# Kernel optimization log

Hardware: AMD Instinct MI355X
Metric: run time of the kernel (lower is better)

## Reference

```python
import jax, jax.numpy as jnp
import numpy as np

B, N, D, H = 32, 2048, 1024, 16
HD = D // H


def setup_inputs() -> dict:
    key = jax.random.key(0)
    ks = jax.random.split(key, 12)
    s = 1.0 / np.sqrt(D)  # xavier-ish scale for square projections
    return {
        "z": jax.random.normal(ks[0], (B, N, D), dtype=jnp.float32),
        "mask": jax.random.bernoulli(ks[1], 0.9, (B, N)),
        "query": jax.random.normal(ks[2], (1, 1, D), dtype=jnp.float32) * s,
        "w_q": jax.random.normal(ks[3], (D, D), dtype=jnp.float32) * s,
        "w_k": jax.random.normal(ks[4], (D, D), dtype=jnp.float32) * s,
        "w_v": jax.random.normal(ks[5], (D, D), dtype=jnp.float32) * s,
        "b_q": jnp.zeros((D,), dtype=jnp.float32),
        "b_k": jnp.zeros((D,), dtype=jnp.float32),
        "b_v": jnp.zeros((D,), dtype=jnp.float32),
        "w_o": jax.random.normal(ks[6], (D, D), dtype=jnp.float32) * s,
        "b_o": jnp.zeros((D,), dtype=jnp.float32),
    }


def reference(z, mask, query, w_q, w_k, w_v, b_q, b_k, b_v, w_o, b_o):
    # mask: True = valid key. Guarantee at least one valid key per row
    # (torch code sets mask[b, 0] = True for all-False rows).
    all_false = ~jnp.any(mask, axis=1)                 # [B]
    valid = mask.at[:, 0].set(mask[:, 0] | all_false)  # [B, N]

    # Projections (PyTorch Linear: x @ W.T + b)
    q = (query @ w_q.T + b_q).reshape(H, HD)           # single shared query -> [H, HD]
    k = (z @ w_k.T + b_k).reshape(B, N, H, HD)
    v = (z @ w_v.T + b_v).reshape(B, N, H, HD)

    scale = 1.0 / jnp.sqrt(jnp.asarray(HD, dtype=z.dtype))
    scores = jnp.einsum('hd,bnhd->bhn', q, k) * scale  # [B, H, N]
    scores = jnp.where(valid[:, None, :], scores, -jnp.inf)
    attn = jax.nn.softmax(scores, axis=-1)             # [B, H, N]

    pooled = jnp.einsum('bhn,bnhd->bhd', attn, v).reshape(B, D)
    return pooled @ w_o.T + b_o                        # [B, D]
```

## Files before the change

### kernel.cpp

```cpp
#include <hip/hip_runtime.h>
#include <hip/hip_bf16.h>
#include <stdint.h>

#define B_ 32
#define N_ 2048
#define D_ 1024
#define H_ 16

#define NT 16
#define RPAD 1028

typedef __attribute__((ext_vector_type(8))) short short8;
typedef __attribute__((ext_vector_type(4))) float f32x4;

__device__ __forceinline__ unsigned short f2bf(float x) {
    unsigned u = __float_as_uint(x);
    u += 0x7FFFu + ((u >> 16) & 1u);
    return (unsigned short)(u >> 16);
}
__device__ __forceinline__ float bflo(unsigned u) { return __uint_as_float(u << 16); }

__device__ __forceinline__ short8 cvt8(float4 a, float4 b) {
    union { __hip_bfloat162 h[4]; short8 s; } u;
    u.h[0] = __float22bfloat162_rn(make_float2(a.x, a.y));
    u.h[1] = __float22bfloat162_rn(make_float2(a.z, a.w));
    u.h[2] = __float22bfloat162_rn(make_float2(b.x, b.y));
    u.h[3] = __float22bfloat162_rn(make_float2(b.z, b.w));
    return u.s;
}

__global__ __launch_bounds__(256) void prep_k(const float* __restrict__ query,
        const float* __restrict__ w_q, const float* __restrict__ b_q,
        const float* __restrict__ w_k, const int* __restrict__ mask,
        unsigned short* __restrict__ rAf, int* __restrict__ any_ws) {
    __shared__ __align__(16) float qv[1024];
    __shared__ float qp[64][5];
    __shared__ float qh[64];
    __shared__ int wf[4];
    int bx = blockIdx.x, t = threadIdx.x;
    if (bx < 64) {
        int h = bx >> 2, dg = bx & 3;
        *(float4*)&qv[4 * t] = *(const float4*)&query[4 * t];
        __syncthreads();
        {
            int j = t >> 2, sub = t & 3;
            const float4* wq4 = (const float4*)(w_q + (size_t)(h * 64 + j) * 1024);
            const float4* qv4 = (const float4*)qv;
            float a = 0.f;
            #pragma unroll 8
            for (int kk = 0; kk < 64; kk++) {
                float4 wv = wq4[sub * 64 + kk];
                float4 vv = qv4[sub * 64 + kk];
                a += wv.x * vv.x + wv.y * vv.y + wv.z * vv.z + wv.w * vv.w;
            }
            qp[j][sub] = a;
        }
        __syncthreads();
        if (t < 64)
            qh[t] = qp[t][0] + qp[t][1] + qp[t][2] + qp[t][3] + b_q[h * 64 + t];
        __syncthreads();
        int d = dg * 256 + t;
        float acc = 0.f;
        #pragma unroll 8
        for (int j = 0; j < 64; j++)
            acc += qh[j] * w_k[(size_t)(h * 64 + j) * 1024 + d];
        acc *= 0.125f;
        int i = d >> 5, fq = (d >> 3) & 3, jj = d & 7;
        int lane = (fq << 4) | h;
        rAf[(size_t)(i * 64 + lane) * 8 + jj] = f2bf(acc);
    } else {
        int b = bx - 64;
        int v = 0;
        for (int k = 0; k < 8; k++) v |= mask[b * N_ + k * 256 + t];
        unsigned long long bal = __ballot(v != 0);
        int w = t >> 6;
        if ((t & 63) == 0) wf[w] = (bal != 0ull) ? 1 : 0;
        __syncthreads();
        if (t == 0) any_ws[b] = wf[0] | wf[1] | wf[2] | wf[3];
    }
}

__global__ __launch_bounds__(256, 1) void main_k(const float* __restrict__ z,
        const int* __restrict__ mask, const int* __restrict__ any_ws,
        const unsigned short* __restrict__ rAf,
        unsigned short* __restrict__ part, float* __restrict__ l_part) {
    __shared__ __align__(16) float zt[2][16 * RPAD];
    __shared__ __align__(16) float Ew[4][16][16];
    int bx = blockIdx.x, t = threadIdx.x;
    int b = bx >> 3, c = bx & 7;
    int n0 = c * 256;
    int w = t >> 6, l = t & 63;
    int frow = l & 15, fquad = l >> 4;
    int anyb = any_ws[b];

    short8 rA[32];
    {
        const short8* rA8 = (const short8*)rAf;
        #pragma unroll
        for (int i = 0; i < 32; i++) rA[i] = rA8[i * 64 + l];
    }
    const float* zb = z + (size_t)b * N_ * D_ + n0 * D_;

    float4 ctx[16];
    #pragma unroll
    for (int h = 0; h < 16; h++) ctx[h] = make_float4(0.f, 0.f, 0.f, 0.f);
    float l4[4] = {0.f, 0.f, 0.f, 0.f};

    #define STAGE(p, tile)                                                        \
        {                                                                         \
            const float* gsrc = zb + (size_t)(tile) * 16 * D_ + w * 256 + l * 4;  \
            float* ldst = &zt[(p)][w * 256];                                      \
            _Pragma("unroll")                                                     \
            for (int r = 0; r < 16; r++) {                                        \
                __builtin_amdgcn_global_load_lds(                                 \
                    (const __attribute__((address_space(1))) unsigned int*)       \
                        (gsrc + (size_t)r * D_),                                  \
                    (__attribute__((address_space(3))) unsigned int*)             \
                        (ldst + r * RPAD),                                        \
                    16, 0, 0);                                                    \
            }                                                                     \
        }

    STAGE(0, 0)
    __syncthreads();

    for (int it = 0; it < NT; it++) {
        int p = it & 1;
        if (it + 1 < NT) STAGE(p ^ 1, it + 1)

        f32x4 a0 = {0.f,0.f,0.f,0.f}, a1 = {0.f,0.f,0.f,0.f};
        f32x4 a2 = {0.f,0.f,0.f,0.f}, a3 = {0.f,0.f,0.f,0.f};
        const float* brow = &zt[p][frow * RPAD + fquad * 8];
        #pragma unroll
        for (int i = 0; i < 32; i += 4) {
            float4 z00 = *(const float4*)(brow + (i + 0) * 32);
            float4 z01 = *(const float4*)(brow + (i + 0) * 32 + 4);
            float4 z10 = *(const float4*)(brow + (i + 1) * 32);
            float4 z11 = *(const float4*)(brow + (i + 1) * 32 + 4);
            float4 z20 = *(const float4*)(brow + (i + 2) * 32);
            float4 z21 = *(const float4*)(brow + (i + 2) * 32 + 4);
            float4 z30 = *(const float4*)(brow + (i + 3) * 32);
            float4 z31 = *(const float4*)(brow + (i + 3) * 32 + 4);
            a0 = __builtin_amdgcn_mfma_f32_16x16x32_bf16(rA[i + 0], cvt8(z00, z01), a0, 0, 0, 0);
            a1 = __builtin_amdgcn_mfma_f32_16x16x32_bf16(rA[i + 1], cvt8(z10, z11), a1, 0, 0, 0);
            a2 = __builtin_amdgcn_mfma_f32_16x16x32_bf16(rA[i + 2], cvt8(z20, z21), a2, 0, 0, 0);
            a3 = __builtin_amdgcn_mfma_f32_16x16x32_bf16(rA[i + 3], cvt8(z30, z31), a3, 0, 0, 0);
        }
        f32x4 acc = a0 + a1 + a2 + a3;

        {
            int gn = n0 + it * 16 + frow;
            bool valid = (mask[b * N_ + gn] != 0) || (gn == 0 && anyb == 0);
            float e0 = valid ? __expf(acc[0]) : 0.f;
            float e1 = valid ? __expf(acc[1]) : 0.f;
            float e2 = valid ? __expf(acc[2]) : 0.f;
            float e3 = valid ? __expf(acc[3]) : 0.f;
            l4[0] += e0; l4[1] += e1; l4[2] += e2; l4[3] += e3;
            *(float4*)&Ew[w][frow][fquad * 4] = make_float4(e0, e1, e2, e3);
        }

        {
            const float* zcol = &zt[p][w * 256 + 4 * l];
            #pragma unroll 4
            for (int r = 0; r < 16; r++) {
                float4 zr = *(const float4*)(zcol + r * RPAD);
                const float4* er4 = (const float4*)&Ew[w][r][0];
                float4 e0 = er4[0], e1 = er4[1], e2 = er4[2], e3 = er4[3];
                ctx[0].x  += e0.x * zr.x; ctx[0].y  += e0.x * zr.y; ctx[0].z  += e0.x * zr.z; ctx[0].w  += e0.x * zr.w;
                ctx[1].x  += e0.y * zr.x; ctx[1].y  += e0.y * zr.y; ctx[1].z  += e0.y * zr.z; ctx[1].w  += e0.y * zr.w;
                ctx[2].x  += e0.z * zr.x; ctx[2].y  += e0.z * zr.y; ctx[2].z  += e0.z * zr.z; ctx[2].w  += e0.z * zr.w;
                ctx[3].x  += e0.w * zr.x; ctx[3].y  += e0.w * zr.y; ctx[3].z  += e0.w * zr.z; ctx[3].w  += e0.w * zr.w;
                ctx[4].x  += e1.x * zr.x; ctx[4].y  += e1.x * zr.y; ctx[4].z  += e1.x * zr.z; ctx[4].w  += e1.x * zr.w;
                ctx[5].x  += e1.y * zr.x; ctx[5].y  += e1.y * zr.y; ctx[5].z  += e1.y * zr.z; ctx[5].w  += e1.y * zr.w;
                ctx[6].x  += e1.z * zr.x; ctx[6].y  += e1.z * zr.y; ctx[6].z  += e1.z * zr.z; ctx[6].w  += e1.z * zr.w;
                ctx[7].x  += e1.w * zr.x; ctx[7].y  += e1.w * zr.y; ctx[7].z  += e1.w * zr.z; ctx[7].w  += e1.w * zr.w;
                ctx[8].x  += e2.x * zr.x; ctx[8].y  += e2.x * zr.y; ctx[8].z  += e2.x * zr.z; ctx[8].w  += e2.x * zr.w;
                ctx[9].x  += e2.y * zr.x; ctx[9].y  += e2.y * zr.y; ctx[9].z  += e2.y * zr.z; ctx[9].w  += e2.y * zr.w;
                ctx[10].x += e2.z * zr.x; ctx[10].y += e2.z * zr.y; ctx[10].z += e2.z * zr.z; ctx[10].w += e2.z * zr.w;
                ctx[11].x += e2.w * zr.x; ctx[11].y += e2.w * zr.y; ctx[11].z += e2.w * zr.z; ctx[11].w += e2.w * zr.w;
                ctx[12].x += e3.x * zr.x; ctx[12].y += e3.x * zr.y; ctx[12].z += e3.x * zr.z; ctx[12].w += e3.x * zr.w;
                ctx[13].x += e3.y * zr.x; ctx[13].y += e3.y * zr.y; ctx[13].z += e3.y * zr.z; ctx[13].w += e3.y * zr.w;
                ctx[14].x += e3.z * zr.x; ctx[14].y += e3.z * zr.y; ctx[14].z += e3.z * zr.z; ctx[14].w += e3.z * zr.w;
                ctx[15].x += e3.w * zr.x; ctx[15].y += e3.w * zr.y; ctx[15].z += e3.w * zr.z; ctx[15].w += e3.w * zr.w;
            }
        }
        __syncthreads();
    }

    {
        unsigned short* pp = part + (size_t)bx * 16 * 1024 + w * 256 + 4 * l;
        #pragma unroll
        for (int h = 0; h < 16; h++) {
            ushort4 o;
            o.x = f2bf(ctx[h].x); o.y = f2bf(ctx[h].y);
            o.z = f2bf(ctx[h].z); o.w = f2bf(ctx[h].w);
            *(ushort4*)(pp + h * 1024) = o;
        }
    }
    if (w == 0) {
        #pragma unroll
        for (int r = 0; r < 4; r++) {
            float v = l4[r];
            v += __shfl_xor(v, 1, 64);
            v += __shfl_xor(v, 2, 64);
            v += __shfl_xor(v, 4, 64);
            v += __shfl_xor(v, 8, 64);
            if (frow == 0) l_part[bx * 16 + fquad * 4 + r] = v;
        }
    }
}

__global__ __launch_bounds__(256) void gemv_wv_k(const unsigned short* __restrict__ part,
        const float* __restrict__ l_part, const float* __restrict__ w_v,
        const float* __restrict__ b_v, float* __restrict__ pooled) {
    __shared__ __align__(16) float vlds[1024];
    int bx = blockIdx.x, t = threadIdx.x;
    int b = bx >> 4, h = bx & 15;
    float L = 0.f;
    #pragma unroll
    for (int cc = 0; cc < 8; cc++) L += l_part[(b * 8 + cc) * 16 + h];
    float rL = 1.f / L;
    float sx = 0.f, sy = 0.f, sz = 0.f, sw = 0.f;
    #pragma unroll
    for (int cc = 0; cc < 8; cc++) {
        const ushort4* p4 = (const ushort4*)&part[(((size_t)(b * 8 + cc)) * 16 + h) * 1024];
        ushort4 u = p4[t];
        sx += bflo(u.x); sy += bflo(u.y); sz += bflo(u.z); sw += bflo(u.w);
    }
    *(float4*)&vlds[4 * t] = make_float4(sx * rL, sy * rL, sz * rL, sw * rL);
    __syncthreads();
    int w = t >> 6, l = t & 63;
    const float4* v4 = (const float4*)vlds;
    float* orow = pooled + (size_t)b * 1024;
    #pragma unroll
    for (int s0 = 0; s0 < 16; s0 += 4) {
        int jb = h * 64 + w * 16 + s0;
        float a0 = 0.f, a1 = 0.f, a2 = 0.f, a3 = 0.f;
        #pragma unroll
        for (int kk = 0; kk < 4; kk++) {
            float4 v = v4[kk * 64 + l];
            float4 w0 = *(const float4*)&w_v[(size_t)(jb + 0) * 1024 + (kk * 64 + l) * 4];
            float4 w1 = *(const float4*)&w_v[(size_t)(jb + 1) * 1024 + (kk * 64 + l) * 4];
            float4 w2 = *(const float4*)&w_v[(size_t)(jb + 2) * 1024 + (kk * 64 + l) * 4];
            float4 w3 = *(const float4*)&w_v[(size_t)(jb + 3) * 1024 + (kk * 64 + l) * 4];
            a0 += w0.x * v.x + w0.y * v.y + w0.z * v.z + w0.w * v.w;
            a1 += w1.x * v.x + w1.y * v.y + w1.z * v.z + w1.w * v.w;
            a2 += w2.x * v.x + w2.y * v.y + w2.z * v.z + w2.w * v.w;
            a3 += w3.x * v.x + w3.y * v.y + w3.z * v.z + w3.w * v.w;
        }
        #pragma unroll
        for (int m = 32; m >= 1; m >>= 1) {
            a0 += __shfl_xor(a0, m, 64); a1 += __shfl_xor(a1, m, 64);
            a2 += __shfl_xor(a2, m, 64); a3 += __shfl_xor(a3, m, 64);
        }
        if (l == 0) {
            orow[jb + 0] = a0 + b_v[jb + 0];
            orow[jb + 1] = a1 + b_v[jb + 1];
            orow[jb + 2] = a2 + b_v[jb + 2];
            orow[jb + 3] = a3 + b_v[jb + 3];
        }
    }
}

__global__ __launch_bounds__(256) void gemv_wo_k(const float* __restrict__ pooled,
        const float* __restrict__ w_o, const float* __restrict__ b_o,
        float* __restrict__ out) {
    __shared__ __align__(16) float vlds[1024];
    int bx = blockIdx.x, t = threadIdx.x;
    int b = bx >> 4, q = bx & 15;
    *(float4*)&vlds[4 * t] = *(const float4*)&pooled[(size_t)b * 1024 + 4 * t];
    __syncthreads();
    int w = t >> 6, l = t & 63;
    const float4* v4 = (const float4*)vlds;
    float* orow = out + (size_t)b * 1024;
    #pragma unroll
    for (int s0 = 0; s0 < 16; s0 += 4) {
        int jb = q * 64 + w * 16 + s0;
        float a0 = 0.f, a1 = 0.f, a2 = 0.f, a3 = 0.f;
        #pragma unroll
        for (int kk = 0; kk < 4; kk++) {
            float4 v = v4[kk * 64 + l];
            float4 w0 = *(const float4*)&w_o[(size_t)(jb + 0) * 1024 + (kk * 64 + l) * 4];
            float4 w1 = *(const float4*)&w_o[(size_t)(jb + 1) * 1024 + (kk * 64 + l) * 4];
            float4 w2 = *(const float4*)&w_o[(size_t)(jb + 2) * 1024 + (kk * 64 + l) * 4];
            float4 w3 = *(const float4*)&w_o[(size_t)(jb + 3) * 1024 + (kk * 64 + l) * 4];
            a0 += w0.x * v.x + w0.y * v.y + w0.z * v.z + w0.w * v.w;
            a1 += w1.x * v.x + w1.y * v.y + w1.z * v.z + w1.w * v.w;
            a2 += w2.x * v.x + w2.y * v.y + w2.z * v.z + w2.w * v.w;
            a3 += w3.x * v.x + w3.y * v.y + w3.z * v.z + w3.w * v.w;
        }
        #pragma unroll
        for (int m = 32; m >= 1; m >>= 1) {
            a0 += __shfl_xor(a0, m, 64); a1 += __shfl_xor(a1, m, 64);
            a2 += __shfl_xor(a2, m, 64); a3 += __shfl_xor(a3, m, 64);
        }
        if (l == 0) {
            orow[jb + 0] = a0 + b_o[jb + 0];
            orow[jb + 1] = a1 + b_o[jb + 1];
            orow[jb + 2] = a2 + b_o[jb + 2];
            orow[jb + 3] = a3 + b_o[jb + 3];
        }
    }
}

extern "C" void kernel_launch(void* const* d_in, const int* in_sizes, int n_in,
                              void* d_out, int out_size, void* d_ws, size_t ws_size,
                              hipStream_t stream) {
    const float* z     = (const float*)d_in[0];
    const int*   mask  = (const int*)d_in[1];
    const float* query = (const float*)d_in[2];
    const float* w_q   = (const float*)d_in[3];
    const float* w_k   = (const float*)d_in[4];
    const float* w_v   = (const float*)d_in[5];
    const float* b_q   = (const float*)d_in[6];
    const float* b_v   = (const float*)d_in[8];
    const float* w_o   = (const float*)d_in[9];
    const float* b_o   = (const float*)d_in[10];
    float* out = (float*)d_out;

    char* ws = (char*)d_ws;
    unsigned short* rAf    = (unsigned short*)(ws + 0);
    int*            any_ws = (int*)(ws + 32768);
    float*          l_part = (float*)(ws + 40960);
    float*          pooled = (float*)(ws + 65536);
    unsigned short* part   = (unsigned short*)(ws + 1048576);

    prep_k<<<96, 256, 0, stream>>>(query, w_q, b_q, w_k, mask, rAf, any_ws);
    main_k<<<256, 256, 0, stream>>>(z, mask, any_ws, rAf, part, l_part);
    gemv_wv_k<<<512, 256, 0, stream>>>(part, l_part, w_v, b_v, pooled);
    gemv_wo_k<<<512, 256, 0, stream>>>(pooled, w_o, b_o, out);
}
```

Baseline: 457.5 us.

## Stage z tiles as bf16 in LDS via register prefetch, double grid occupancy

Replaces the direct global-to-LDS fp32 staging with register-held global loads that are converted to bf16 once and written to LDS in three chunks interleaved with the MFMA and context phases. This halves the LDS footprint, so two blocks fit per CU, and the grid doubles to 512 blocks of 128 keys each. Mask values are also cached in LDS, and the downstream gemv reduces over 16 partials instead of 8. The cost is higher register pressure from the prefetch buffers, plus bf16 rounding of z in the value-weighted sum, which was fp32 before.

```diff
diff --git a/kernel.cpp b/kernel.cpp
--- a/kernel.cpp
+++ b/kernel.cpp
@@ -7,8 +7,8 @@
 #define D_ 1024
 #define H_ 16
 
-#define NT 16
-#define RPAD 1028
+#define NT 8
+#define RPB 1032
 
 typedef __attribute__((ext_vector_type(8))) short short8;
 typedef __attribute__((ext_vector_type(4))) float f32x4;
@@ -80,15 +80,16 @@
     }
 }
 
-__global__ __launch_bounds__(256, 1) void main_k(const float* __restrict__ z,
+__global__ __launch_bounds__(256, 2) void main_k(const float* __restrict__ z,
         const int* __restrict__ mask, const int* __restrict__ any_ws,
         const unsigned short* __restrict__ rAf,
         unsigned short* __restrict__ part, float* __restrict__ l_part) {
-    __shared__ __align__(16) float zt[2][16 * RPAD];
-    __shared__ __align__(16) float Ew[4][16][16];
+    __shared__ __align__(16) unsigned short ztb[2][16 * RPB];
+    __shared__ __align__(16) float Ew[4][16][20];
+    __shared__ int mlds[128];
     int bx = blockIdx.x, t = threadIdx.x;
-    int b = bx >> 3, c = bx & 7;
-    int n0 = c * 256;
+    int b = bx >> 4, c = bx & 15;
+    int n0 = c * 128;
     int w = t >> 6, l = t & 63;
     int frow = l & 15, fquad = l >> 4;
     int anyb = any_ws[b];
@@ -99,58 +100,81 @@
         #pragma unroll
         for (int i = 0; i < 32; i++) rA[i] = rA8[i * 64 + l];
     }
-    const float* zb = z + (size_t)b * N_ * D_ + n0 * D_;
+    const float* zb = z + (size_t)b * N_ * D_ + (size_t)n0 * D_;
+
+    if (t < 128) mlds[t] = mask[b * N_ + n0 + t];
 
     float4 ctx[16];
     #pragma unroll
     for (int h = 0; h < 16; h++) ctx[h] = make_float4(0.f, 0.f, 0.f, 0.f);
     float l4[4] = {0.f, 0.f, 0.f, 0.f};
 
-    #define STAGE(p, tile)                                                        \
+    float4 ga[4], gb[4], gc[8];
+    #define ISSUE4(g, tile, rb)                                                   \
         {                                                                         \
-            const float* gsrc = zb + (size_t)(tile) * 16 * D_ + w * 256 + l * 4;  \
-            float* ldst = &zt[(p)][w * 256];                                      \
-            _Pragma("unroll")                                                     \
-            for (int r = 0; r < 16; r++) {                                        \
-                __builtin_amdgcn_global_load_lds(                                 \
-                    (const __attribute__((address_space(1))) unsigned int*)       \
-                        (gsrc + (size_t)r * D_),                                  \
-                    (__attribute__((address_space(3))) unsigned int*)             \
-                        (ldst + r * RPAD),                                        \
-                    16, 0, 0);                                                    \
-            }                                                                     \
-        }
-
-    STAGE(0, 0)
+            const float4* src = (const float4*)(zb + (size_t)(tile) * 16 * D_ +   \
+                                                (size_t)((rb) + w) * D_);         \
+            g[0] = src[2 * l];       g[1] = src[2 * l + 1];                       \
+            g[2] = src[2 * (l + 64)]; g[3] = src[2 * (l + 64) + 1];               \
+        }
+    #define WRITE4(g, pp, rb)                                                     \
+        {                                                                         \
+            unsigned short* dst = &ztb[(pp)][((rb) + w) * RPB];                   \
+            *(short8*)(dst + l * 8) = cvt8(g[0], g[1]);                           \
+            *(short8*)(dst + (l + 64) * 8) = cvt8(g[2], g[3]);                    \
+        }
+    #define ISSUE8(g, tile)                                                       \
+        {                                                                         \
+            const float4* s0 = (const float4*)(zb + (size_t)(tile) * 16 * D_ +    \
+                                               (size_t)(8 + 2 * w) * D_);         \
+            const float4* s1 = (const float4*)(zb + (size_t)(tile) * 16 * D_ +    \
+                                               (size_t)(9 + 2 * w) * D_);         \
+            g[0] = s0[2 * l];       g[1] = s0[2 * l + 1];                         \
+            g[2] = s0[2 * (l + 64)]; g[3] = s0[2 * (l + 64) + 1];                 \
+            g[4] = s1[2 * l];       g[5] = s1[2 * l + 1];                         \
+            g[6] = s1[2 * (l + 64)]; g[7] = s1[2 * (l + 64) + 1];                 \
+        }
+    #define WRITE8(g, pp)                                                         \
+        {                                                                         \
+            unsigned short* d0 = &ztb[(pp)][(8 + 2 * w) * RPB];                   \
+            unsigned short* d1 = &ztb[(pp)][(9 + 2 * w) * RPB];                   \
+            *(short8*)(d0 + l * 8) = cvt8(g[0], g[1]);                            \
+            *(short8*)(d0 + (l + 64) * 8) = cvt8(g[2], g[3]);                     \
+            *(short8*)(d1 + l * 8) = cvt8(g[4], g[5]);                            \
+            *(short8*)(d1 + (l + 64) * 8) = cvt8(g[6], g[7]);                     \
+        }
+
+    ISSUE4(ga, 0, 0)  WRITE4(ga, 0, 0)
+    ISSUE4(gb, 0, 4)  WRITE4(gb, 0, 4)
+    ISSUE8(gc, 0)     WRITE8(gc, 0)
     __syncthreads();
 
     for (int it = 0; it < NT; it++) {
         int p = it & 1;
-        if (it + 1 < NT) STAGE(p ^ 1, it + 1)
+        bool nx = (it + 1 < NT);
+        if (nx) ISSUE4(ga, it + 1, 0)
 
         f32x4 a0 = {0.f,0.f,0.f,0.f}, a1 = {0.f,0.f,0.f,0.f};
         f32x4 a2 = {0.f,0.f,0.f,0.f}, a3 = {0.f,0.f,0.f,0.f};
-        const float* brow = &zt[p][frow * RPAD + fquad * 8];
+        const unsigned short* brow = &ztb[p][frow * RPB + fquad * 8];
         #pragma unroll
         for (int i = 0; i < 32; i += 4) {
-            float4 z00 = *(const float4*)(brow + (i + 0) * 32);
-            float4 z01 = *(const float4*)(brow + (i + 0) * 32 + 4);
-            float4 z10 = *(const float4*)(brow + (i + 1) * 32);
-            float4 z11 = *(const float4*)(brow + (i + 1) * 32 + 4);
-            float4 z20 = *(const float4*)(brow + (i + 2) * 32);
-            float4 z21 = *(const float4*)(brow + (i + 2) * 32 + 4);
-            float4 z30 = *(const float4*)(brow + (i + 3) * 32);
-            float4 z31 = *(const float4*)(brow + (i + 3) * 32 + 4);
-            a0 = __builtin_amdgcn_mfma_f32_16x16x32_bf16(rA[i + 0], cvt8(z00, z01), a0, 0, 0, 0);
-            a1 = __builtin_amdgcn_mfma_f32_16x16x32_bf16(rA[i + 1], cvt8(z10, z11), a1, 0, 0, 0);
-            a2 = __builtin_amdgcn_mfma_f32_16x16x32_bf16(rA[i + 2], cvt8(z20, z21), a2, 0, 0, 0);
-            a3 = __builtin_amdgcn_mfma_f32_16x16x32_bf16(rA[i + 3], cvt8(z30, z31), a3, 0, 0, 0);
+            short8 b0 = *(const short8*)(brow + (i + 0) * 32);
+            short8 b1 = *(const short8*)(brow + (i + 1) * 32);
+            short8 b2 = *(const short8*)(brow + (i + 2) * 32);
+            short8 b3 = *(const short8*)(brow + (i + 3) * 32);
+            a0 = __builtin_amdgcn_mfma_f32_16x16x32_bf16(rA[i + 0], b0, a0, 0, 0, 0);
+            a1 = __builtin_amdgcn_mfma_f32_16x16x32_bf16(rA[i + 1], b1, a1, 0, 0, 0);
+            a2 = __builtin_amdgcn_mfma_f32_16x16x32_bf16(rA[i + 2], b2, a2, 0, 0, 0);
+            a3 = __builtin_amdgcn_mfma_f32_16x16x32_bf16(rA[i + 3], b3, a3, 0, 0, 0);
         }
         f32x4 acc = a0 + a1 + a2 + a3;
+
+        if (nx) { WRITE4(ga, p ^ 1, 0)  ISSUE4(gb, it + 1, 4) }
 
         {
             int gn = n0 + it * 16 + frow;
-            bool valid = (mask[b * N_ + gn] != 0) || (gn == 0 && anyb == 0);
+            bool valid = (mlds[it * 16 + frow] != 0) || (gn == 0 && anyb == 0);
             float e0 = valid ? __expf(acc[0]) : 0.f;
             float e1 = valid ? __expf(acc[1]) : 0.f;
             float e2 = valid ? __expf(acc[2]) : 0.f;
@@ -159,31 +183,37 @@
             *(float4*)&Ew[w][frow][fquad * 4] = make_float4(e0, e1, e2, e3);
         }
 
-        {
-            const float* zcol = &zt[p][w * 256 + 4 * l];
-            #pragma unroll 4
-            for (int r = 0; r < 16; r++) {
-                float4 zr = *(const float4*)(zcol + r * RPAD);
-                const float4* er4 = (const float4*)&Ew[w][r][0];
-                float4 e0 = er4[0], e1 = er4[1], e2 = er4[2], e3 = er4[3];
-                ctx[0].x  += e0.x * zr.x; ctx[0].y  += e0.x * zr.y; ctx[0].z  += e0.x * zr.z; ctx[0].w  += e0.x * zr.w;
-                ctx[1].x  += e0.y * zr.x; ctx[1].y  += e0.y * zr.y; ctx[1].z  += e0.y * zr.z; ctx[1].w  += e0.y * zr.w;
-                ctx[2].x  += e0.z * zr.x; ctx[2].y  += e0.z * zr.y; ctx[2].z  += e0.z * zr.z; ctx[2].w  += e0.z * zr.w;
-                ctx[3].x  += e0.w * zr.x; ctx[3].y  += e0.w * zr.y; ctx[3].z  += e0.w * zr.z; ctx[3].w  += e0.w * zr.w;
-                ctx[4].x  += e1.x * zr.x; ctx[4].y  += e1.x * zr.y; ctx[4].z  += e1.x * zr.z; ctx[4].w  += e1.x * zr.w;
-                ctx[5].x  += e1.y * zr.x; ctx[5].y  += e1.y * zr.y; ctx[5].z  += e1.y * zr.z; ctx[5].w  += e1.y * zr.w;
-                ctx[6].x  += e1.z * zr.x; ctx[6].y  += e1.z * zr.y; ctx[6].z  += e1.z * zr.z; ctx[6].w  += e1.z * zr.w;
-                ctx[7].x  += e1.w * zr.x; ctx[7].y  += e1.w * zr.y; ctx[7].z  += e1.w * zr.z; ctx[7].w  += e1.w * zr.w;
-                ctx[8].x  += e2.x * zr.x; ctx[8].y  += e2.x * zr.y; ctx[8].z  += e2.x * zr.z; ctx[8].w  += e2.x * zr.w;
-                ctx[9].x  += e2.y * zr.x; ctx[9].y  += e2.y * zr.y; ctx[9].z  += e2.y * zr.z; ctx[9].w  += e2.y * zr.w;
-                ctx[10].x += e2.z * zr.x; ctx[10].y += e2.z * zr.y; ctx[10].z += e2.z * zr.z; ctx[10].w += e2.z * zr.w;
-                ctx[11].x += e2.w * zr.x; ctx[11].y += e2.w * zr.y; ctx[11].z += e2.w * zr.z; ctx[11].w += e2.w * zr.w;
-                ctx[12].x += e3.x * zr.x; ctx[12].y += e3.x * zr.y; ctx[12].z += e3.x * zr.z; ctx[12].w += e3.x * zr.w;
-                ctx[13].x += e3.y * zr.x; ctx[13].y += e3.y * zr.y; ctx[13].z += e3.y * zr.z; ctx[13].w += e3.y * zr.w;
-                ctx[14].x += e3.z * zr.x; ctx[14].y += e3.z * zr.y; ctx[14].z += e3.z * zr.z; ctx[14].w += e3.z * zr.w;
-                ctx[15].x += e3.w * zr.x; ctx[15].y += e3.w * zr.y; ctx[15].z += e3.w * zr.z; ctx[15].w += e3.w * zr.w;
+        const unsigned short* zcol = &ztb[p][w * 256 + 4 * l];
+        #define CTXROW(r)                                                         \
+            {                                                                     \
+                ushort4 u = *(const ushort4*)(zcol + (r) * RPB);                  \
+                float zx = bflo(u.x), zy = bflo(u.y);                             \
+                float zz = bflo(u.z), zw = bflo(u.w);                             \
+                const float4* er4 = (const float4*)&Ew[w][(r)][0];                \
+                float4 e0 = er4[0], e1 = er4[1], e2 = er4[2], e3 = er4[3];        \
+                ctx[0].x  += e0.x * zx; ctx[0].y  += e0.x * zy; ctx[0].z  += e0.x * zz; ctx[0].w  += e0.x * zw; \
+                ctx[1].x  += e0.y * zx; ctx[1].y  += e0.y * zy; ctx[1].z  += e0.y * zz; ctx[1].w  += e0.y * zw; \
+                ctx[2].x  += e0.z * zx; ctx[2].y  += e0.z * zy; ctx[2].z  += e0.z * zz; ctx[2].w  += e0.z * zw; \
+                ctx[3].x  += e0.w * zx; ctx[3].y  += e0.w * zy; ctx[3].z  += e0.w * zz; ctx[3].w  += e0.w * zw; \
+                ctx[4].x  += e1.x * zx; ctx[4].y  += e1.x * zy; ctx[4].z  += e1.x * zz; ctx[4].w  += e1.x * zw; \
+                ctx[5].x  += e1.y * zx; ctx[5].y  += e1.y * zy; ctx[5].z  += e1.y * zz; ctx[5].w  += e1.y * zw; \
+                ctx[6].x  += e1.z * zx; ctx[6].y  += e1.z * zy; ctx[6].z  += e1.z * zz; ctx[6].w  += e1.z * zw; \
+                ctx[7].x  += e1.w * zx; ctx[7].y  += e1.w * zy; ctx[7].z  += e1.w * zz; ctx[7].w  += e1.w * zw; \
+                ctx[8].x  += e2.x * zx; ctx[8].y  += e2.x * zy; ctx[8].z  += e2.x * zz; ctx[8].w  += e2.x * zw; \
+                ctx[9].x  += e2.y * zx; ctx[9].y  += e2.y * zy; ctx[9].z  += e2.y * zz; ctx[9].w  += e2.y * zw; \
+                ctx[10].x += e2.z * zx; ctx[10].y += e2.z * zy; ctx[10].z += e2.z * zz; ctx[10].w += e2.z * zw; \
+                ctx[11].x += e2.w * zx; ctx[11].y += e2.w * zy; ctx[11].z += e2.w * zz; ctx[11].w += e2.w * zw; \
+                ctx[12].x += e3.x * zx; ctx[12].y += e3.x * zy; ctx[12].z += e3.x * zz; ctx[12].w += e3.x * zw; \
+                ctx[13].x += e3.y * zx; ctx[13].y += e3.y * zy; ctx[13].z += e3.y * zz; ctx[13].w += e3.y * zw; \
+                ctx[14].x += e3.z * zx; ctx[14].y += e3.z * zy; ctx[14].z += e3.z * zz; ctx[14].w += e3.z * zw; \
+                ctx[15].x += e3.w * zx; ctx[15].y += e3.w * zy; ctx[15].z += e3.w * zz; ctx[15].w += e3.w * zw; \
             }
-        }
+        #pragma unroll
+        for (int r = 0; r < 8; r++) CTXROW(r)
+        if (nx) { WRITE4(gb, p ^ 1, 4)  ISSUE8(gc, it + 1) }
+        #pragma unroll
+        for (int r = 8; r < 16; r++) CTXROW(r)
+        if (nx) WRITE8(gc, p ^ 1)
         __syncthreads();
     }
 
@@ -218,12 +248,12 @@
     int b = bx >> 4, h = bx & 15;
     float L = 0.f;
     #pragma unroll
-    for (int cc = 0; cc < 8; cc++) L += l_part[(b * 8 + cc) * 16 + h];
+    for (int cc = 0; cc < 16; cc++) L += l_part[(b * 16 + cc) * 16 + h];
     float rL = 1.f / L;
     float sx = 0.f, sy = 0.f, sz = 0.f, sw = 0.f;
     #pragma unroll
-    for (int cc = 0; cc < 8; cc++) {
-        const ushort4* p4 = (const ushort4*)&part[(((size_t)(b * 8 + cc)) * 16 + h) * 1024];
+    for (int cc = 0; cc < 16; cc++) {
+        const ushort4* p4 = (const ushort4*)&part[(((size_t)(b * 16 + cc)) * 16 + h) * 1024];
         ushort4 u = p4[t];
         sx += bflo(u.x); sy += bflo(u.y); sz += bflo(u.z); sw += bflo(u.w);
     }
@@ -321,12 +351,12 @@
     char* ws = (char*)d_ws;
     unsigned short* rAf    = (unsigned short*)(ws + 0);
     int*            any_ws = (int*)(ws + 32768);
-    float*          l_part = (float*)(ws + 40960);
-    float*          pooled = (float*)(ws + 65536);
+    float*          l_part = (float*)(ws + 36864);
+    float*          pooled = (float*)(ws + 131072);
     unsigned short* part   = (unsigned short*)(ws + 1048576);
 
     prep_k<<<96, 256, 0, stream>>>(query, w_q, b_q, w_k, mask, rAf, any_ws);
-    main_k<<<256, 256, 0, stream>>>(z, mask, any_ws, rAf, part, l_part);
+    main_k<<<512, 256, 0, stream>>>(z, mask, any_ws, rAf, part, l_part);
     gemv_wv_k<<<512, 256, 0, stream>>>(part, l_part, w_v, b_v, pooled);
     gemv_wo_k<<<512, 256, 0, stream>>>(pooled, w_o, b_o, out);
 }
```

New measurement: 902.0 us. 1.97x slower.

## Double main kernel waves to split context accumulation and cache mask in LDS

Applied to the files above, without the earlier changes.

The main attention kernel goes from 256 to 512 threads per block, so each wave accumulates the weighted context over 128 feature columns instead of 256. This halves the per-thread FMA work and the register footprint of the context accumulators. The staging loop is remapped so each wave copies two full rows of the z tile, and the per-block mask slice is preloaded into shared memory instead of being read from global memory every iteration. In exchange, every wave still computes the full score MFMA redundantly, so that work doubles per block. The tighter launch bound also risks register spills, given the 32 resident bf16 query fragments.

```diff
diff --git a/kernel.cpp b/kernel.cpp
--- a/kernel.cpp
+++ b/kernel.cpp
@@ -80,12 +80,13 @@
     }
 }
 
-__global__ __launch_bounds__(256, 1) void main_k(const float* __restrict__ z,
+__global__ __launch_bounds__(512, 2) void main_k(const float* __restrict__ z,
         const int* __restrict__ mask, const int* __restrict__ any_ws,
         const unsigned short* __restrict__ rAf,
         unsigned short* __restrict__ part, float* __restrict__ l_part) {
     __shared__ __align__(16) float zt[2][16 * RPAD];
-    __shared__ __align__(16) float Ew[4][16][16];
+    __shared__ __align__(16) float Ew[8][16][16];
+    __shared__ int mlds[256];
     int bx = blockIdx.x, t = threadIdx.x;
     int b = bx >> 3, c = bx & 7;
     int n0 = c * 256;
@@ -99,25 +100,32 @@
         #pragma unroll
         for (int i = 0; i < 32; i++) rA[i] = rA8[i * 64 + l];
     }
-    const float* zb = z + (size_t)b * N_ * D_ + n0 * D_;
-
-    float4 ctx[16];
-    #pragma unroll
-    for (int h = 0; h < 16; h++) ctx[h] = make_float4(0.f, 0.f, 0.f, 0.f);
+    const float* zb = z + (size_t)b * N_ * D_ + (size_t)n0 * D_;
+
+    if (t < 256) mlds[t] = mask[b * N_ + n0 + t];
+
+    float2 ctx[16];
+    #pragma unroll
+    for (int h = 0; h < 16; h++) ctx[h] = make_float2(0.f, 0.f);
     float l4[4] = {0.f, 0.f, 0.f, 0.f};
 
     #define STAGE(p, tile)                                                        \
         {                                                                         \
-            const float* gsrc = zb + (size_t)(tile) * 16 * D_ + w * 256 + l * 4;  \
-            float* ldst = &zt[(p)][w * 256];                                      \
             _Pragma("unroll")                                                     \
-            for (int r = 0; r < 16; r++) {                                        \
-                __builtin_amdgcn_global_load_lds(                                 \
-                    (const __attribute__((address_space(1))) unsigned int*)       \
-                        (gsrc + (size_t)r * D_),                                  \
-                    (__attribute__((address_space(3))) unsigned int*)             \
-                        (ldst + r * RPAD),                                        \
-                    16, 0, 0);                                                    \
+            for (int rr = 0; rr < 2; rr++) {                                      \
+                int row = 2 * w + rr;                                             \
+                const float* gsrc = zb + (size_t)(tile) * 16 * D_ +               \
+                                    (size_t)row * D_ + l * 4;                     \
+                float* ldst = &zt[(p)][row * RPAD];                               \
+                _Pragma("unroll")                                                 \
+                for (int q = 0; q < 4; q++) {                                     \
+                    __builtin_amdgcn_global_load_lds(                             \
+                        (const __attribute__((address_space(1))) unsigned int*)   \
+                            (gsrc + q * 256),                                     \
+                        (__attribute__((address_space(3))) unsigned int*)         \
+                            (ldst + q * 256),                                     \
+                        16, 0, 0);                                                \
+                }                                                                 \
             }                                                                     \
         }
 
@@ -150,7 +158,7 @@
 
         {
             int gn = n0 + it * 16 + frow;
-            bool valid = (mask[b * N_ + gn] != 0) || (gn == 0 && anyb == 0);
+            bool valid = (mlds[it * 16 + frow] != 0) || (gn == 0 && anyb == 0);
             float e0 = valid ? __expf(acc[0]) : 0.f;
             float e1 = valid ? __expf(acc[1]) : 0.f;
             float e2 = valid ? __expf(acc[2]) : 0.f;
@@ -160,41 +168,40 @@
         }
 
         {
-            const float* zcol = &zt[p][w * 256 + 4 * l];
+            const float* zcol = &zt[p][w * 128 + 2 * l];
             #pragma unroll 4
             for (int r = 0; r < 16; r++) {
-                float4 zr = *(const float4*)(zcol + r * RPAD);
+                float2 zr = *(const float2*)(zcol + r * RPAD);
                 const float4* er4 = (const float4*)&Ew[w][r][0];
                 float4 e0 = er4[0], e1 = er4[1], e2 = er4[2], e3 = er4[3];
-                ctx[0].x  += e0.x * zr.x; ctx[0].y  += e0.x * zr.y; ctx[0].z  += e0.x * zr.z; ctx[0].w  += e0.x * zr.w;
-                ctx[1].x  += e0.y * zr.x; ctx[1].y  += e0.y * zr.y; ctx[1].z  += e0.y * zr.z; ctx[1].w  += e0.y * zr.w;
-                ctx[2].x  += e0.z * zr.x; ctx[2].y  += e0.z * zr.y; ctx[2].z  += e0.z * zr.z; ctx[2].w  += e0.z * zr.w;
-                ctx[3].x  += e0.w * zr.x; ctx[3].y  += e0.w * zr.y; ctx[3].z  += e0.w * zr.z; ctx[3].w  += e0.w * zr.w;
-                ctx[4].x  += e1.x * zr.x; ctx[4].y  += e1.x * zr.y; ctx[4].z  += e1.x * zr.z; ctx[4].w  += e1.x * zr.w;
-                ctx[5].x  += e1.y * zr.x; ctx[5].y  += e1.y * zr.y; ctx[5].z  += e1.y * zr.z; ctx[5].w  += e1.y * zr.w;
-                ctx[6].x  += e1.z * zr.x; ctx[6].y  += e1.z * zr.y; ctx[6].z  += e1.z * zr.z; ctx[6].w  += e1.z * zr.w;
-                ctx[7].x  += e1.w * zr.x; ctx[7].y  += e1.w * zr.y; ctx[7].z  += e1.w * zr.z; ctx[7].w  += e1.w * zr.w;
-                ctx[8].x  += e2.x * zr.x; ctx[8].y  += e2.x * zr.y; ctx[8].z  += e2.x * zr.z; ctx[8].w  += e2.x * zr.w;
-                ctx[9].x  += e2.y * zr.x; ctx[9].y  += e2.y * zr.y; ctx[9].z  += e2.y * zr.z; ctx[9].w  += e2.y * zr.w;
-                ctx[10].x += e2.z * zr.x; ctx[10].y += e2.z * zr.y; ctx[10].z += e2.z * zr.z; ctx[10].w += e2.z * zr.w;
-                ctx[11].x += e2.w * zr.x; ctx[11].y += e2.w * zr.y; ctx[11].z += e2.w * zr.z; ctx[11].w += e2.w * zr.w;
-                ctx[12].x += e3.x * zr.x; ctx[12].y += e3.x * zr.y; ctx[12].z += e3.x * zr.z; ctx[12].w += e3.x * zr.w;
-                ctx[13].x += e3.y * zr.x; ctx[13].y += e3.y * zr.y; ctx[13].z += e3.y * zr.z; ctx[13].w += e3.y * zr.w;
-                ctx[14].x += e3.z * zr.x; ctx[14].y += e3.z * zr.y; ctx[14].z += e3.z * zr.z; ctx[14].w += e3.z * zr.w;
-                ctx[15].x += e3.w * zr.x; ctx[15].y += e3.w * zr.y; ctx[15].z += e3.w * zr.z; ctx[15].w += e3.w * zr.w;
+                ctx[0].x  += e0.x * zr.x; ctx[0].y  += e0.x * zr.y;
+                ctx[1].x  += e0.y * zr.x; ctx[1].y  += e0.y * zr.y;
+                ctx[2].x  += e0.z * zr.x; ctx[2].y  += e0.z * zr.y;
+                ctx[3].x  += e0.w * zr.x; ctx[3].y  += e0.w * zr.y;
+                ctx[4].x  += e1.x * zr.x; ctx[4].y  += e1.x * zr.y;
+                ctx[5].x  += e1.y * zr.x; ctx[5].y  += e1.y * zr.y;
+                ctx[6].x  += e1.z * zr.x; ctx[6].y  += e1.z * zr.y;
+                ctx[7].x  += e1.w * zr.x; ctx[7].y  += e1.w * zr.y;
+                ctx[8].x  += e2.x * zr.x; ctx[8].y  += e2.x * zr.y;
+                ctx[9].x  += e2.y * zr.x; ctx[9].y  += e2.y * zr.y;
+                ctx[10].x += e2.z * zr.x; ctx[10].y += e2.z * zr.y;
+                ctx[11].x += e2.w * zr.x; ctx[11].y += e2.w * zr.y;
+                ctx[12].x += e3.x * zr.x; ctx[12].y += e3.x * zr.y;
+                ctx[13].x += e3.y * zr.x; ctx[13].y += e3.y * zr.y;
+                ctx[14].x += e3.z * zr.x; ctx[14].y += e3.z * zr.y;
+                ctx[15].x += e3.w * zr.x; ctx[15].y += e3.w * zr.y;
             }
         }
         __syncthreads();
     }
 
     {
-        unsigned short* pp = part + (size_t)bx * 16 * 1024 + w * 256 + 4 * l;
+        unsigned short* pp = part + (size_t)bx * 16 * 1024 + w * 128 + 2 * l;
         #pragma unroll
         for (int h = 0; h < 16; h++) {
-            ushort4 o;
+            ushort2 o;
             o.x = f2bf(ctx[h].x); o.y = f2bf(ctx[h].y);
-            o.z = f2bf(ctx[h].z); o.w = f2bf(ctx[h].w);
-            *(ushort4*)(pp + h * 1024) = o;
+            *(ushort2*)(pp + h * 1024) = o;
         }
     }
     if (w == 0) {
@@ -326,7 +333,7 @@
     unsigned short* part   = (unsigned short*)(ws + 1048576);
 
     prep_k<<<96, 256, 0, stream>>>(query, w_q, b_q, w_k, mask, rAf, any_ws);
-    main_k<<<256, 256, 0, stream>>>(z, mask, any_ws, rAf, part, l_part);
+    main_k<<<256, 512, 0, stream>>>(z, mask, any_ws, rAf, part, l_part);
     gemv_wv_k<<<512, 256, 0, stream>>>(part, l_part, w_v, b_v, pooled);
     gemv_wo_k<<<512, 256, 0, stream>>>(pooled, w_o, b_o, out);
 }
```

Measured after the change: 494.4 us. 1.08x slower.
